# Kernel tuning notes

Measured on AMD Instinct MI355X. Metric: run time of the kernel, lower is better.

## Reference

```python
import jax, jax.numpy as jnp
import numpy as np

B, S, E, H = 2, 2048, 1024, 16
D = E // H

def setup_inputs() -> dict:
    key = jax.random.key(0)
    k1, k2, k3, k4, k5 = jax.random.split(key, 5)
    s = 1.0 / np.sqrt(E)
    return {
        "x": jax.random.normal(k1, (B, S, E), dtype=jnp.float32),
        "wv_w": jax.random.uniform(k2, (E, E), jnp.float32, -s, s),
        "wv_b": jax.random.uniform(k3, (E,), jnp.float32, -s, s),
        "wo_w": jax.random.uniform(k4, (E, E), jnp.float32, -s, s),
        "wo_b": jax.random.uniform(k5, (E,), jnp.float32, -s, s),
    }

def reference(x, wv_w, wv_b, wo_w, wo_b):
    b, s_len, e = x.shape
    # v projection -> (B, H, S, D)
    v = (x @ wv_w.T + wv_b).reshape(b, s_len, H, D).transpose(0, 2, 1, 3)
    # causal mask: True above diagonal (blocked); m = inclusive lower triangle
    causal = jnp.triu(jnp.ones((s_len, s_len), dtype=bool), k=1)
    m = (~causal).astype(x.dtype)
    # per-batch min-max scaling over (h, s, d)
    v_min = v.min(axis=(1, 2, 3), keepdims=True)
    v_max = v.max(axis=(1, 2, 3), keepdims=True)
    v_scaled = (v - v_min) / (v_max - v_min + 1e-8)
    # genetic fitness: masked mean pooling + reciprocal-mean normalization
    summed = jnp.einsum('ij,bhjd->bhid', m, v_scaled)  # (B,H,S,D)
    counts = jnp.maximum(m.sum(axis=1), 1.0)[None, None, :, None]
    phi = summed / counts
    denom = phi + 0.5
    sum_inv = (1.0 / denom).sum(axis=-1, keepdims=True)
    gene_fitness = 1.0 / (denom * sum_inv)  # weight, (B,H,S,D)
    # organism fitness scores
    org = jnp.einsum('bhjd,bhid->bhij', v_scaled, gene_fitness)
    org = jnp.where(causal[None, None], -jnp.inf, org)
    attn = jax.nn.softmax(org, axis=-1)
    out = jnp.einsum('bhij,bhjd->bhid', attn, v)
    out = out.transpose(0, 2, 1, 3).reshape(b, s_len, e)
    return out @ wo_w.T + wo_b
```

## Files before the change

### kernel.cpp

```cpp
#include <hip/hip_runtime.h>
#include <hip/hip_bf16.h>

#define B_ 2
#define S_ 2048
#define E_ 1024
#define H_ 16
#define D_ 64
#define M_ 4096

typedef __bf16 bf16_t;
typedef bf16_t bf16x8 __attribute__((ext_vector_type(8)));
typedef float f32x4 __attribute__((ext_vector_type(4)));
typedef unsigned int u32;

__device__ __forceinline__ f32x4 mfma16(bf16x8 a, bf16x8 b, f32x4 c) {
    return __builtin_amdgcn_mfma_f32_16x16x32_bf16(a, b, c, 0, 0, 0);
}
__device__ __forceinline__ unsigned short f2bf(float f) {
    unsigned int u = __float_as_uint(f);
    unsigned int r = (u + 0x7fffu + ((u >> 16) & 1u)) >> 16;
    return (unsigned short)r;
}
__device__ __forceinline__ float bf2f(unsigned short s) {
    return __uint_as_float(((unsigned int)s) << 16);
}
__device__ __forceinline__ u32 cvt_pk_bf16(float lo, float hi) {
    u32 r;
    asm("v_cvt_pk_bf16_f32 %0, %1, %2" : "=v"(r) : "v"(lo), "v"(hi));
    return r;
}
__device__ __forceinline__ unsigned int fenc(float x) {
    unsigned int u = __float_as_uint(x);
    return (u & 0x80000000u) ? ~u : (u | 0x80000000u);
}
__device__ __forceinline__ float fdec(unsigned int u) {
    return __uint_as_float((u & 0x80000000u) ? (u ^ 0x80000000u) : ~u);
}
__device__ __forceinline__ void gload16(const void* g, void* l) {
    __builtin_amdgcn_global_load_lds((const __attribute__((address_space(1))) u32*)g,
                                     (__attribute__((address_space(3))) u32*)l, 16, 0, 0);
}

__global__ void k_init(unsigned int* mm) {
    int t = threadIdx.x;
    if (t < 2) { mm[t * 2] = 0xFFFFFFFFu; mm[t * 2 + 1] = 0u; }
}

__global__ __launch_bounds__(256) void k_cast(const float* __restrict__ src,
                                              unsigned short* __restrict__ dst, int n8) {
    int i = blockIdx.x * 256 + threadIdx.x;
    if (i >= n8) return;
    const float4* s4 = (const float4*)src;
    float4 a = s4[2 * i], c = s4[2 * i + 1];
    uint4 o;
    o.x = cvt_pk_bf16(a.x, a.y);
    o.y = cvt_pk_bf16(a.z, a.w);
    o.z = cvt_pk_bf16(c.x, c.y);
    o.w = cvt_pk_bf16(c.z, c.w);
    ((uint4*)dst)[i] = o;
}

template <int MODE>
__global__ __launch_bounds__(256, 2) void k_gemm(const unsigned short* __restrict__ A,
                                                 const unsigned short* __restrict__ Bm,
                                                 const float* __restrict__ bias,
                                                 unsigned short* __restrict__ outb,
                                                 unsigned short* __restrict__ vtb,
                                                 float* __restrict__ outf,
                                                 unsigned int* __restrict__ mm) {
    __shared__ __align__(16) unsigned short Asm[2][8192];
    __shared__ __align__(16) unsigned short Bsm[2][8192];
    const int K = 1024;
    int tid = threadIdx.x, lane = tid & 63, wv = tid >> 6;
    int wm = wv >> 1, wn = wv & 1;
    int m0 = blockIdx.x * 128, n0 = blockIdx.y * 128;
    int lrow = lane & 15, lgrp = lane >> 4, sw = lane & 7;
    int r8 = lane >> 3, ch = lane & 7;
    const unsigned short* Ag = A + (size_t)(m0 + wv * 8 + r8) * K + ((ch ^ r8) << 3);
    const unsigned short* Bg = Bm + (size_t)(n0 + wv * 8 + r8) * K + ((ch ^ r8) << 3);

#define STAGE(buf, kk)                                                                     \
    {                                                                                      \
        _Pragma("unroll") for (int i = 0; i < 4; ++i)                                      \
            gload16(Ag + (size_t)(i * 32) * K + (kk), &Asm[buf][(i * 32 + wv * 8) * 64]);  \
        _Pragma("unroll") for (int i = 0; i < 4; ++i)                                      \
            gload16(Bg + (size_t)(i * 32) * K + (kk), &Bsm[buf][(i * 32 + wv * 8) * 64]);  \
    }
#define COMPUTE(buf)                                                                        \
    {                                                                                       \
        _Pragma("unroll") for (int kh = 0; kh < 2; ++kh) {                                  \
            int cp = (((kh << 2) | lgrp) ^ sw) << 3;                                        \
            bf16x8 af[4], bfr[4];                                                           \
            _Pragma("unroll") for (int mt = 0; mt < 4; ++mt)                                \
                af[mt] = *(const bf16x8*)&Asm[buf][(wm * 64 + mt * 16 + lrow) * 64 + cp];   \
            _Pragma("unroll") for (int nt = 0; nt < 4; ++nt)                                \
                bfr[nt] = *(const bf16x8*)&Bsm[buf][(wn * 64 + nt * 16 + lrow) * 64 + cp];  \
            _Pragma("unroll") for (int mt = 0; mt < 4; ++mt)                                \
                _Pragma("unroll") for (int nt = 0; nt < 4; ++nt)                            \
                    acc[mt][nt] = mfma16(af[mt], bfr[nt], acc[mt][nt]);                     \
        }                                                                                   \
    }

    f32x4 acc[4][4];
#pragma unroll
    for (int i = 0; i < 4; ++i)
#pragma unroll
        for (int j = 0; j < 4; ++j) acc[i][j] = (f32x4){0.f, 0.f, 0.f, 0.f};

    STAGE(0, 0);
    for (int t = 0; t < 16; ++t) {
        asm volatile("s_waitcnt vmcnt(0)" ::: "memory");
        __builtin_amdgcn_s_barrier();
        __builtin_amdgcn_sched_barrier(0);
        if (t + 1 < 16) STAGE((t + 1) & 1, (t + 1) * 64);
        __builtin_amdgcn_s_setprio(1);
        COMPUTE(t & 1);
        __builtin_amdgcn_s_setprio(0);
    }
#undef STAGE
#undef COMPUTE

    float vmin = 1e30f, vmax = -1e30f;
#pragma unroll
    for (int nt = 0; nt < 4; ++nt) {
        int ncol = n0 + wn * 64 + nt * 16 + lrow;
        float bs = bias[ncol];
#pragma unroll
        for (int mt = 0; mt < 4; ++mt) {
            unsigned int lo = 0, hi = 0;
#pragma unroll
            for (int r = 0; r < 4; ++r) {
                int mrow = m0 + wm * 64 + mt * 16 + lgrp * 4 + r;
                float val = acc[mt][nt][r] + bs;
                if constexpr (MODE == 0) {
                    vmin = fminf(vmin, val);
                    vmax = fmaxf(vmax, val);
                    int b = mrow >> 11, s = mrow & 2047, h = ncol >> 6, d = ncol & 63;
                    unsigned short bfv = f2bf(val);
                    outb[(size_t)((b * 16 + h) * 2048 + s) * 64 + d] = bfv;
                    if (r < 2) lo |= ((unsigned int)bfv) << (16 * r);
                    else       hi |= ((unsigned int)bfv) << (16 * (r - 2));
                } else {
                    outf[(size_t)mrow * 1024 + ncol] = val;
                }
            }
            if constexpr (MODE == 0) {
                int mrow0 = m0 + wm * 64 + mt * 16 + lgrp * 4;
                int b = mrow0 >> 11, s0 = mrow0 & 2047;
                int h = ncol >> 6, d = ncol & 63;
                uint2 pk; pk.x = lo; pk.y = hi;
                *(uint2*)&vtb[((size_t)(b * 16 + h) * 64 + d) * 2048 + s0] = pk;
            }
        }
    }
    if constexpr (MODE == 0) {
#pragma unroll
        for (int m = 1; m < 64; m <<= 1) {
            vmin = fminf(vmin, __shfl_xor(vmin, m));
            vmax = fmaxf(vmax, __shfl_xor(vmax, m));
        }
        if (lane == 0) {
            int b = m0 >> 11;
            atomicMin(&mm[b * 2], fenc(vmin));
            atomicMax(&mm[b * 2 + 1], fenc(vmax));
        }
    }
}

__global__ __launch_bounds__(256) void k_scan1(const unsigned short* __restrict__ vb,
                                               float* __restrict__ ps) {
    int g = blockIdx.x * 4 + (threadIdx.x >> 6);
    int d = threadIdx.x & 63;
    int bh = g >> 6, c = g & 63;
    const unsigned short* src = vb + (size_t)bh * S_ * 64 + (size_t)c * 32 * 64 + d;
    float a0 = 0.f, a1 = 0.f, a2 = 0.f, a3 = 0.f;
#pragma unroll
    for (int i = 0; i < 32; i += 4) {
        a0 += bf2f(src[(size_t)i * 64]);
        a1 += bf2f(src[(size_t)(i + 1) * 64]);
        a2 += bf2f(src[(size_t)(i + 2) * 64]);
        a3 += bf2f(src[(size_t)(i + 3) * 64]);
    }
    ps[(size_t)g * 64 + d] = (a0 + a1) + (a2 + a3);
}

__global__ __launch_bounds__(64) void k_scan2(const float* __restrict__ ps,
                                              float* __restrict__ base) {
    int bh = blockIdx.x;
    int d = threadIdx.x;
    const float* p = ps + (size_t)bh * 64 * 64 + d;
    float* bo = base + (size_t)bh * 64 * 64 + d;
    float vals[64];
#pragma unroll
    for (int c = 0; c < 64; ++c) vals[c] = p[(size_t)c * 64];
    float run = 0.f;
#pragma unroll
    for (int c = 0; c < 64; ++c) {
        float t = vals[c];
        vals[c] = run;
        run += t;
    }
#pragma unroll
    for (int c = 0; c < 64; ++c) bo[(size_t)c * 64] = vals[c];
}

__global__ __launch_bounds__(256) void k_scan3(const unsigned short* __restrict__ vb,
                                               const float* __restrict__ base,
                                               unsigned short* __restrict__ gene,
                                               const unsigned int* __restrict__ mm) {
    int g = blockIdx.x * 4 + (threadIdx.x >> 6);
    int d = threadIdx.x & 63;
    int bh = g >> 6, c = g & 63;
    int b = bh >> 4;
    float vmin = fdec(mm[b * 2]), vmax = fdec(mm[b * 2 + 1]);
    float ir = __fdividef(1.0f, vmax - vmin + 1e-8f);
    float irl = ir * 1.4426950408889634f;
    const unsigned short* src = vb + (size_t)bh * S_ * 64 + (size_t)c * 32 * 64 + d;
    unsigned short* dst = gene + (size_t)bh * S_ * 64 + (size_t)c * 32 * 64 + d;
    float acc = base[(size_t)g * 64 + d];
#pragma unroll 4
    for (int i = 0; i < 32; ++i) {
        int s = c * 32 + i;
        acc += bf2f(src[(size_t)i * 64]);
        float phi = __fdividef(acc, (float)(s + 1));
        float inv = __fdividef(1.0f, (phi - vmin) * ir + 0.5f);
        float rs = inv;
#pragma unroll
        for (int m = 1; m < 64; m <<= 1) rs += __shfl_xor(rs, m);
        dst[(size_t)i * 64] = f2bf(__fdividef(inv, rs) * irl);
    }
}

__global__ __launch_bounds__(256, 4) void k_attn(const unsigned short* __restrict__ gene,
                                                 const unsigned short* __restrict__ vb,
                                                 const unsigned short* __restrict__ vt,
                                                 unsigned short* __restrict__ attn_out,
                                                 const unsigned int* __restrict__ mm) {
    __shared__ __align__(16) unsigned short Vsm[2][4096];
    __shared__ __align__(16) unsigned short Tsm[2][4096];
    __shared__ __align__(16) unsigned short plds[4][1024];
    int tid = threadIdx.x, lane = tid & 63, w = tid >> 6;
    int bid = blockIdx.x;
    int qt = 31 - (bid >> 5);
    int bh = ((bid & 7) << 2) | ((bid >> 3) & 3);
    int i0 = qt * 64 + w * 16;
    int lrow = lane & 15, lgrp = lane >> 4;
    int sx = lrow & 7;
    int r8 = lane >> 3, ch = lane & 7;

    int b = bh >> 4;
    float vmin = fdec(mm[b * 2]), vmax = fdec(mm[b * 2 + 1]);
    float ir = __fdividef(1.0f, vmax - vmin + 1e-8f);
    float C2 = (vmin * ir + 1.0f) * 1.4426950408889634f;

    const unsigned short* gbase = gene + (size_t)bh * S_ * 64;
    const unsigned short* vbase = vb + (size_t)bh * S_ * 64;
    const unsigned short* tbase = vt + (size_t)bh * 64 * S_;

    const unsigned short* Vg = vbase + (size_t)(w * 8 + r8) * 64 + ((ch ^ r8) << 3);
    const unsigned short* Tg = tbase + (size_t)(w * 8 + r8) * S_ + ((ch ^ r8) << 3);

#define ASTAGE(buf, jt_)                                                                  \
    {                                                                                     \
        int j0s = (jt_) << 6;                                                             \
        _Pragma("unroll") for (int i = 0; i < 2; ++i)                                     \
            gload16(Vg + (size_t)(j0s + i * 32) * 64, &Vsm[buf][(i * 32 + w * 8) * 64]);  \
        _Pragma("unroll") for (int i = 0; i < 2; ++i)                                     \
            gload16(Tg + (size_t)(i * 32) * S_ + j0s, &Tsm[buf][(i * 32 + w * 8) * 64]);  \
    }

    bf16x8 ga0 = *(const bf16x8*)(gbase + (size_t)(i0 + lrow) * 64 + lgrp * 8);
    bf16x8 ga1 = *(const bf16x8*)(gbase + (size_t)(i0 + lrow) * 64 + 32 + lgrp * 8);

    f32x4 acc[4];
#pragma unroll
    for (int dn = 0; dn < 4; ++dn) acc[dn] = (f32x4){0.f, 0.f, 0.f, 0.f};
    float lsum = 0.f;

    int njt = qt + 1;
    ASTAGE(0, 0);
    for (int jt = 0; jt < njt; ++jt) {
        int cur = jt & 1;
        asm volatile("s_waitcnt vmcnt(0)" ::: "memory");
        __builtin_amdgcn_s_barrier();
        __builtin_amdgcn_sched_barrier(0);
        if (jt + 1 < njt) ASTAGE(cur ^ 1, jt + 1);
        int j0 = jt << 6;
        __builtin_amdgcn_s_setprio(1);
        f32x4 Sv[4];
#pragma unroll
        for (int n = 0; n < 4; ++n) {
            const unsigned short* vr = &Vsm[cur][(n * 16 + lrow) * 64];
            bf16x8 a0 = *(const bf16x8*)(vr + ((lgrp ^ sx) << 3));
            bf16x8 a1 = *(const bf16x8*)(vr + (((lgrp + 4) ^ sx) << 3));
            f32x4 c = (f32x4){0.f, 0.f, 0.f, 0.f};
            c = mfma16(a0, ga0, c);
            c = mfma16(a1, ga1, c);
            Sv[n] = c;
        }
        bool tail = (jt == njt - 1);
#pragma unroll
        for (int n = 0; n < 4; ++n) {
            float q0 = exp2f(Sv[n][0] - C2);
            float q1 = exp2f(Sv[n][1] - C2);
            float q2 = exp2f(Sv[n][2] - C2);
            float q3 = exp2f(Sv[n][3] - C2);
            if (tail) {
                int ii = i0 + lrow;
                int jj = j0 + n * 16 + 4 * lgrp;
                q0 = (jj     <= ii) ? q0 : 0.f;
                q1 = (jj + 1 <= ii) ? q1 : 0.f;
                q2 = (jj + 2 <= ii) ? q2 : 0.f;
                q3 = (jj + 3 <= ii) ? q3 : 0.f;
            }
            lsum += (q0 + q1) + (q2 + q3);
            uint2 pk;
            pk.x = cvt_pk_bf16(q0, q1);
            pk.y = cvt_pk_bf16(q2, q3);
            int chunk = 2 * n + (lgrp >> 1);
            *(uint2*)&plds[w][lrow * 64 + ((chunk ^ sx) << 3) + ((lgrp & 1) << 2)] = pk;
        }
#pragma unroll
        for (int chk = 0; chk < 2; ++chk) {
            int pc = ((chk * 4 + lgrp) ^ sx) << 3;
            bf16x8 pa = *(const bf16x8*)&plds[w][lrow * 64 + pc];
#pragma unroll
            for (int dn = 0; dn < 4; ++dn) {
                bf16x8 tf = *(const bf16x8*)&Tsm[cur][(dn * 16 + lrow) * 64 + pc];
                acc[dn] = mfma16(tf, pa, acc[dn]);
            }
        }
        __builtin_amdgcn_s_setprio(0);
    }
#undef ASTAGE
    lsum += __shfl_xor(lsum, 16);
    lsum += __shfl_xor(lsum, 32);
    lsum = __fdividef(1.0f, lsum);
    int bb = bh >> 4, h = bh & 15;
    int ii = i0 + lrow;
#pragma unroll
    for (int dn = 0; dn < 4; ++dn) {
        uint2 pk;
        pk.x = cvt_pk_bf16(acc[dn][0] * lsum, acc[dn][1] * lsum);
        pk.y = cvt_pk_bf16(acc[dn][2] * lsum, acc[dn][3] * lsum);
        int e = h * 64 + dn * 16 + lgrp * 4;
        *(uint2*)&attn_out[(size_t)(bb * S_ + ii) * E_ + e] = pk;
    }
}

extern "C" void kernel_launch(void* const* d_in, const int* in_sizes, int n_in,
                              void* d_out, int out_size, void* d_ws, size_t ws_size,
                              hipStream_t stream) {
    const float* x = (const float*)d_in[0];
    const float* wv_w = (const float*)d_in[1];
    const float* wv_b = (const float*)d_in[2];
    const float* wo_w = (const float*)d_in[3];
    const float* wo_b = (const float*)d_in[4];
    float* out = (float*)d_out;

    char* w = (char*)d_ws;
    unsigned short* x_bf = (unsigned short*)(w);
    unsigned short* wv_bf = (unsigned short*)(w + 8388608);
    unsigned short* wo_bf = (unsigned short*)(w + 10485760);
    unsigned short* v_bf = (unsigned short*)(w + 12582912);
    unsigned short* vt_bf = (unsigned short*)(w + 20971520);
    float* ps = (float*)(w + 29360128);
    float* base = (float*)(w + 29884416);
    unsigned short* gene = (unsigned short*)(w + 46137344);
    unsigned short* a_bf = (unsigned short*)(w + 54525952);
    unsigned int* mm = (unsigned int*)(w + 62914560);
    if (ws_size < 62914576) return;

    k_init<<<1, 64, 0, stream>>>(mm);
    k_cast<<<2048, 256, 0, stream>>>(x, x_bf, 524288);
    k_cast<<<512, 256, 0, stream>>>(wv_w, wv_bf, 131072);
    k_cast<<<512, 256, 0, stream>>>(wo_w, wo_bf, 131072);
    k_gemm<0><<<dim3(32, 8), 256, 0, stream>>>(x_bf, wv_bf, wv_b, v_bf, vt_bf, nullptr, mm);
    k_scan1<<<512, 256, 0, stream>>>(v_bf, ps);
    k_scan2<<<32, 64, 0, stream>>>(ps, base);
    k_scan3<<<512, 256, 0, stream>>>(v_bf, base, gene, mm);
    k_attn<<<1024, 256, 0, stream>>>(gene, v_bf, vt_bf, a_bf, mm);
    k_gemm<1><<<dim3(32, 8), 256, 0, stream>>>(a_bf, wo_bf, wo_b, nullptr, nullptr, out, nullptr);
}
```

Measured before the change: 141.3 us.

## Load GEMM B operand directly into registers and deepen A prefetch

The B operand tiles now go straight from global memory into registers, double-buffered one k-step ahead, instead of through shared memory. The A operand keeps its shared-memory path but is now prefetched two stages ahead, with a second barrier after compute. This removes the B shared-memory traffic and halves LDS usage, which could help occupancy. In exchange it raises register pressure (two 8-vector B buffers per thread), uses uncoalesced-ish 16-byte global loads per lane for B, and adds a second barrier per iteration.

```diff
diff --git a/kernel.cpp b/kernel.cpp
--- a/kernel.cpp
+++ b/kernel.cpp
@@ -69,7 +69,6 @@
                                                  float* __restrict__ outf,
                                                  unsigned int* __restrict__ mm) {
     __shared__ __align__(16) unsigned short Asm[2][8192];
-    __shared__ __align__(16) unsigned short Bsm[2][8192];
     const int K = 1024;
     int tid = threadIdx.x, lane = tid & 63, wv = tid >> 6;
     int wm = wv >> 1, wn = wv & 1;
@@ -77,28 +76,19 @@
     int lrow = lane & 15, lgrp = lane >> 4, sw = lane & 7;
     int r8 = lane >> 3, ch = lane & 7;
     const unsigned short* Ag = A + (size_t)(m0 + wv * 8 + r8) * K + ((ch ^ r8) << 3);
-    const unsigned short* Bg = Bm + (size_t)(n0 + wv * 8 + r8) * K + ((ch ^ r8) << 3);
-
-#define STAGE(buf, kk)                                                                     \
+    const unsigned short* Bgr = Bm + (size_t)(n0 + wn * 64 + lrow) * K + lgrp * 8;
+
+#define STAGE_A(buf, kk)                                                                   \
     {                                                                                      \
         _Pragma("unroll") for (int i = 0; i < 4; ++i)                                      \
             gload16(Ag + (size_t)(i * 32) * K + (kk), &Asm[buf][(i * 32 + wv * 8) * 64]);  \
-        _Pragma("unroll") for (int i = 0; i < 4; ++i)                                      \
-            gload16(Bg + (size_t)(i * 32) * K + (kk), &Bsm[buf][(i * 32 + wv * 8) * 64]);  \
-    }
-#define COMPUTE(buf)                                                                        \
-    {                                                                                       \
-        _Pragma("unroll") for (int kh = 0; kh < 2; ++kh) {                                  \
-            int cp = (((kh << 2) | lgrp) ^ sw) << 3;                                        \
-            bf16x8 af[4], bfr[4];                                                           \
-            _Pragma("unroll") for (int mt = 0; mt < 4; ++mt)                                \
-                af[mt] = *(const bf16x8*)&Asm[buf][(wm * 64 + mt * 16 + lrow) * 64 + cp];   \
-            _Pragma("unroll") for (int nt = 0; nt < 4; ++nt)                                \
-                bfr[nt] = *(const bf16x8*)&Bsm[buf][(wn * 64 + nt * 16 + lrow) * 64 + cp];  \
-            _Pragma("unroll") for (int mt = 0; mt < 4; ++mt)                                \
-                _Pragma("unroll") for (int nt = 0; nt < 4; ++nt)                            \
-                    acc[mt][nt] = mfma16(af[mt], bfr[nt], acc[mt][nt]);                     \
-        }                                                                                   \
+    }
+#define LOADB(dst, tt)                                                                     \
+    {                                                                                      \
+        _Pragma("unroll") for (int nt = 0; nt < 4; ++nt)                                   \
+            _Pragma("unroll") for (int kh = 0; kh < 2; ++kh)                               \
+                (dst)[nt * 2 + kh] =                                                       \
+                    *(const bf16x8*)(Bgr + (size_t)(nt * 16) * K + (tt) * 64 + kh * 32);   \
     }
 
     f32x4 acc[4][4];
@@ -107,18 +97,42 @@
 #pragma unroll
         for (int j = 0; j < 4; ++j) acc[i][j] = (f32x4){0.f, 0.f, 0.f, 0.f};
 
-    STAGE(0, 0);
+    bf16x8 breg[2][8];
+    LOADB(breg[0], 0);
+    STAGE_A(0, 0);
+    STAGE_A(1, 64);
+#pragma unroll
     for (int t = 0; t < 16; ++t) {
-        asm volatile("s_waitcnt vmcnt(0)" ::: "memory");
+        if (t < 15) LOADB(breg[(t + 1) & 1], t + 1);
+        if (t < 15) {
+            asm volatile("s_waitcnt vmcnt(12)" ::: "memory");
+        } else {
+            asm volatile("s_waitcnt vmcnt(0)" ::: "memory");
+        }
         __builtin_amdgcn_s_barrier();
         __builtin_amdgcn_sched_barrier(0);
-        if (t + 1 < 16) STAGE((t + 1) & 1, (t + 1) * 64);
         __builtin_amdgcn_s_setprio(1);
-        COMPUTE(t & 1);
+#pragma unroll
+        for (int kh = 0; kh < 2; ++kh) {
+            int cp = (((kh << 2) | lgrp) ^ sw) << 3;
+            bf16x8 af[4];
+#pragma unroll
+            for (int mt = 0; mt < 4; ++mt)
+                af[mt] = *(const bf16x8*)&Asm[t & 1][(wm * 64 + mt * 16 + lrow) * 64 + cp];
+#pragma unroll
+            for (int mt = 0; mt < 4; ++mt)
+#pragma unroll
+                for (int nt = 0; nt < 4; ++nt)
+                    acc[mt][nt] = mfma16(af[mt], breg[t & 1][nt * 2 + kh], acc[mt][nt]);
+        }
         __builtin_amdgcn_s_setprio(0);
-    }
-#undef STAGE
-#undef COMPUTE
+        asm volatile("s_waitcnt lgkmcnt(0)" ::: "memory");
+        __builtin_amdgcn_s_barrier();
+        __builtin_amdgcn_sched_barrier(0);
+        if (t < 14) STAGE_A(t & 1, (t + 2) * 64);
+    }
+#undef STAGE_A
+#undef LOADB
 
     float vmin = 1e30f, vmax = -1e30f;
 #pragma unroll
```

New measurement: 152.3 us. 1.08x slower.
